# Performance work log

Measured on AMD Instinct MI355X. Metric: run time of the kernel, lower is better.

Reference implementation:

```python
import jax, jax.numpy as jnp
import numpy as np

IN_CH = 2048
OUT_CH = 2048
BATCH = 8192


def setup_inputs() -> dict:
    key = jax.random.key(0)
    ks = jax.random.split(key, 8)
    bound = 1.0 / np.sqrt(IN_CH)  # torch nn.Linear default init range
    inp = {
        "input": jax.random.normal(ks[0], (BATCH, IN_CH), dtype=jnp.float32),
        "hidden": jax.random.normal(ks[1], (BATCH, OUT_CH), dtype=jnp.float32),
        "cell": jax.random.normal(ks[2], (BATCH, OUT_CH), dtype=jnp.float32),
        # Fused gate weights: [IN_CH, 4*OUT_CH] for (forget, input, output, state)
        "W": jax.random.uniform(ks[3], (IN_CH, 4 * OUT_CH), minval=-bound, maxval=bound, dtype=jnp.float32),
        "b": jax.random.uniform(ks[4], (4 * OUT_CH,), minval=-bound, maxval=bound, dtype=jnp.float32),
    }
    return inp


def reference(input, hidden, cell, W, b):
    # One fused GEMM for all four gates, then fused elementwise gate math.
    gates = input @ W + b  # [B, 4*OUT_CH]
    f_g, i_g, o_g, s_g = jnp.split(gates, 4, axis=-1)
    # NOTE: original module applies sigmoid (not tanh) to the state gate.
    forget_gate = jax.nn.sigmoid(f_g)
    input_gate = jax.nn.sigmoid(i_g)
    output_gate = jax.nn.sigmoid(o_g)
    state_gate = jax.nn.sigmoid(s_g)
    new_cell = forget_gate * cell + input_gate * state_gate
    new_hidden = output_gate * jnp.tanh(new_cell)
    return (new_hidden, new_cell)
```

## Files before the change

kernel.cpp:

```cpp
#include <hip/hip_runtime.h>
#include <cstddef>
#include <cstdint>

#define B_ROWS 8192
#define K_DIM  2048
#define N_GATE 2048
#define NG     4
#define W_COLS (NG * N_GATE)

#define BM   256
#define BK   64
#define NTIL 32

typedef __attribute__((ext_vector_type(8))) short s16x8;
typedef __attribute__((ext_vector_type(4))) float f32x4;

__device__ __forceinline__ float fast_sigmoid(float x) {
  return 1.0f / (1.0f + __expf(-x));
}
__device__ __forceinline__ float fast_tanh(float x) {
  return 1.0f - 2.0f / (__expf(2.0f * x) + 1.0f);
}

__global__ void convert_in_kernel(const float4* __restrict__ src,
                                  s16x8* __restrict__ dst, int n8) {
  int idx = blockIdx.x * blockDim.x + threadIdx.x;
  int stride = gridDim.x * blockDim.x;
  for (int i = idx; i < n8; i += stride) {
    float4 a = src[2 * i], b = src[2 * i + 1];
    s16x8 o = { __builtin_bit_cast(short, (__bf16)a.x),
                __builtin_bit_cast(short, (__bf16)a.y),
                __builtin_bit_cast(short, (__bf16)a.z),
                __builtin_bit_cast(short, (__bf16)a.w),
                __builtin_bit_cast(short, (__bf16)b.x),
                __builtin_bit_cast(short, (__bf16)b.y),
                __builtin_bit_cast(short, (__bf16)b.z),
                __builtin_bit_cast(short, (__bf16)b.w) };
    dst[i] = o;
  }
}

__device__ __forceinline__ unsigned int pack2bf16(float x, float y) {
  unsigned short lo = __builtin_bit_cast(unsigned short, (__bf16)x);
  unsigned short hi = __builtin_bit_cast(unsigned short, (__bf16)y);
  return ((unsigned int)hi << 16) | lo;
}

__global__ __launch_bounds__(256) void convert_w_kernel(const float* __restrict__ W,
                                                        short* __restrict__ Wt) {
  __shared__ unsigned int tile[64 * 32];
  const int t = threadIdx.x;
  const int n0 = blockIdx.x * 64;
  const int k0 = blockIdx.y * 64;
  {
    const int kr = t >> 2, seg = t & 3;
    const float4* src = (const float4*)(W + (size_t)(k0 + kr) * W_COLS + n0 + seg * 16);
#pragma unroll
    for (int u = 0; u < 4; ++u) {
      float4 v = src[u];
      const int np = seg * 8 + u * 2;
      tile[kr * 32 + (np ^ (kr & 31))]       = pack2bf16(v.x, v.y);
      tile[kr * 32 + ((np + 1) ^ (kr & 31))] = pack2bf16(v.z, v.w);
    }
  }
  __syncthreads();
  {
    const int np = t >> 3;
    const int kb = t & 7;
    unsigned int w[8];
#pragma unroll
    for (int v = 0; v < 8; ++v) {
      const int k = kb * 8 + v;
      w[v] = tile[k * 32 + (np ^ (k & 31))];
    }
    s16x8 lo, hi;
#pragma unroll
    for (int v = 0; v < 8; ++v) {
      lo[v] = (short)(w[v] & 0xffff);
      hi[v] = (short)(w[v] >> 16);
    }
    short* d0 = Wt + (size_t)(n0 + 2 * np) * K_DIM + k0 + kb * 8;
    *(s16x8*)d0 = lo;
    *(s16x8*)(d0 + K_DIM) = hi;
  }
}

#define GL16(gsrc, ldst)                                                        \
  __builtin_amdgcn_global_load_lds(                                             \
      (const __attribute__((address_space(1))) unsigned int*)(gsrc),            \
      (__attribute__((address_space(3))) unsigned int*)(ldst), 16, 0, 0)

#define MFMA16 __builtin_amdgcn_mfma_f32_16x16x32_bf16

__global__ __launch_bounds__(512, 2) void lstm_gemm_kernel(
    const short* __restrict__ Abf,
    const short* __restrict__ Wt,
    const float* __restrict__ bias,
    const float* __restrict__ cell,
    float* __restrict__ outH,
    float* __restrict__ outC) {
  extern __shared__ short lds[];

  const int tid = threadIdx.x;
  const int lane = tid & 63;
  const int wid = tid >> 6;
  const int wm = wid >> 2;
  const int wn = wid & 3;
  const int lrow = lane & 15;
  const int lk = lane >> 4;

  const int bid = blockIdx.x;
  const int xcd = bid & 7, j = bid >> 3;
  const int tn = xcd * 4 + (j >> 5);
  const int tm = j & 31;
  const int m0 = tm * BM;
  const int n0 = tn * 64;

  size_t a_src[2][2], b_src[2][2];
#pragma unroll
  for (int h = 0; h < 2; ++h)
#pragma unroll
    for (int jj = 0; jj < 2; ++jj) {
      const int p = h * 1024 + jj * 512 + tid;
      const int r = p >> 3;
      const int gl = (p & 7) ^ (r & 7);
      a_src[h][jj] = (size_t)(m0 + r) * K_DIM + gl * 8;
      const int wn16 = r >> 6, g = (r >> 4) & 3, nc4 = r & 15;
      b_src[h][jj] = (size_t)(g * N_GATE + n0 + wn16 * 16 + nc4) * K_DIM + gl * 8;
    }

#define STAGE_A(BUF, H, KT) do {                                                 \
    GL16(Abf + a_src[H][0] + (size_t)(KT) * BK,                                  \
         lds + (BUF) * 16384 + ((H) * 1024 + tid) * 8);                          \
    GL16(Abf + a_src[H][1] + (size_t)(KT) * BK,                                  \
         lds + (BUF) * 16384 + ((H) * 1024 + 512 + tid) * 8);                    \
  } while (0)
#define STAGE_B(BUF, H, KT) do {                                                 \
    GL16(Wt + b_src[H][0] + (size_t)(KT) * BK,                                   \
         lds + 32768 + (BUF) * 16384 + ((H) * 1024 + tid) * 8);                  \
    GL16(Wt + b_src[H][1] + (size_t)(KT) * BK,                                   \
         lds + 32768 + (BUF) * 16384 + ((H) * 1024 + 512 + tid) * 8);            \
  } while (0)

  const int pg0 = (lk ^ (lrow & 7)) * 16;
  const int pg1 = ((4 + lk) ^ (lrow & 7)) * 16;
  const char* aK0 = (const char*)lds + (wm * 128 + lrow) * 128 + pg0;
  const char* aK1 = (const char*)lds + (wm * 128 + lrow) * 128 + pg1;
  const char* bK0 = (const char*)lds + 65536 + (wn * 64 + lrow) * 128 + pg0;
  const char* bK1 = (const char*)lds + 65536 + (wn * 64 + lrow) * 128 + pg1;
#define AF(BUF, MI, KK) (*(const s16x8*)(aK##KK + (BUF) * 32768 + (MI) * 2048))
#define BFR(BUF, G, KK) (*(const s16x8*)(bK##KK + (BUF) * 32768 + (G) * 2048))

  f32x4 acc[8][4];
#pragma unroll
  for (int mi = 0; mi < 8; ++mi)
#pragma unroll
    for (int g = 0; g < 4; ++g) acc[mi][g] = (f32x4){0.f, 0.f, 0.f, 0.f};

  s16x8 bfr[4][2];

#define MMQ(MI, A0, A1) do {                                                     \
    acc[MI][0] = MFMA16(A0, bfr[0][0], acc[MI][0], 0, 0, 0);                     \
    acc[MI][0] = MFMA16(A1, bfr[0][1], acc[MI][0], 0, 0, 0);                     \
    acc[MI][1] = MFMA16(A0, bfr[1][0], acc[MI][1], 0, 0, 0);                     \
    acc[MI][1] = MFMA16(A1, bfr[1][1], acc[MI][1], 0, 0, 0);                     \
    acc[MI][2] = MFMA16(A0, bfr[2][0], acc[MI][2], 0, 0, 0);                     \
    acc[MI][2] = MFMA16(A1, bfr[2][1], acc[MI][2], 0, 0, 0);                     \
    acc[MI][3] = MFMA16(A0, bfr[3][0], acc[MI][3], 0, 0, 0);                     \
    acc[MI][3] = MFMA16(A1, bfr[3][1], acc[MI][3], 0, 0, 0);                     \
  } while (0)

#define VM_NONE do {} while (0)
#define VM_4 asm volatile("s_waitcnt vmcnt(4)" ::: "memory")
#define VM_0 asm volatile("s_waitcnt vmcnt(0)" ::: "memory")

#define PHASE(BUF, Q, LOADB, STG, VM) do {                                       \
    if (LOADB) {                                                                 \
      bfr[0][0] = BFR(BUF, 0, 0); bfr[0][1] = BFR(BUF, 0, 1);                    \
      bfr[1][0] = BFR(BUF, 1, 0); bfr[1][1] = BFR(BUF, 1, 1);                    \
      bfr[2][0] = BFR(BUF, 2, 0); bfr[2][1] = BFR(BUF, 2, 1);                    \
      bfr[3][0] = BFR(BUF, 3, 0); bfr[3][1] = BFR(BUF, 3, 1);                    \
    }                                                                            \
    s16x8 af00 = AF(BUF, 2 * (Q), 0), af01 = AF(BUF, 2 * (Q), 1);                \
    s16x8 af10 = AF(BUF, 2 * (Q) + 1, 0), af11 = AF(BUF, 2 * (Q) + 1, 1);        \
    STG;                                                                         \
    VM;                                                                          \
    __builtin_amdgcn_s_barrier();                                                \
    asm volatile("s_waitcnt lgkmcnt(0)" ::: "memory");                           \
    __builtin_amdgcn_s_setprio(1);                                               \
    MMQ(2 * (Q), af00, af01);                                                    \
    MMQ(2 * (Q) + 1, af10, af11);                                                \
    __builtin_amdgcn_s_setprio(0);                                               \
    __builtin_amdgcn_s_barrier();                                                \
  } while (0)

  STAGE_B(0, 0, 0); STAGE_B(0, 1, 0); STAGE_A(0, 0, 0); STAGE_A(0, 1, 0);
  STAGE_B(1, 0, 1); STAGE_B(1, 1, 1);
  VM_4;
  __builtin_amdgcn_s_barrier();

  for (int i = 0; i < NTIL / 2 - 1; ++i) {
    const int t1 = 2 * i + 1, t2 = 2 * i + 2, t3 = 2 * i + 3;
    PHASE(0, 0, 1, { STAGE_A(1, 0, t1); }, VM_NONE);
    PHASE(0, 1, 0, { STAGE_A(1, 1, t1); }, VM_NONE);
    PHASE(0, 2, 0, { STAGE_B(0, 0, t2); }, VM_NONE);
    PHASE(0, 3, 0, { STAGE_B(0, 1, t2); }, VM_4);
    PHASE(1, 0, 1, { STAGE_A(0, 0, t2); }, VM_NONE);
    PHASE(1, 1, 0, { STAGE_A(0, 1, t2); }, VM_NONE);
    PHASE(1, 2, 0, { STAGE_B(1, 0, t3); }, VM_NONE);
    PHASE(1, 3, 0, { STAGE_B(1, 1, t3); }, VM_4);
  }

  PHASE(0, 0, 1, { STAGE_A(1, 0, 31); }, VM_NONE);
  PHASE(0, 1, 0, { STAGE_A(1, 1, 31); }, VM_NONE);
  PHASE(0, 2, 0, {}, VM_NONE);
  PHASE(0, 3, 0, {}, VM_0);
  PHASE(1, 0, 1, {}, VM_NONE);
  PHASE(1, 1, 0, {}, VM_NONE);
  PHASE(1, 2, 0, {}, VM_NONE);
  PHASE(1, 3, 0, {}, VM_NONE);

  {
    const int n = n0 + wn * 16 + lrow;
    const float b0 = bias[n];
    const float b1 = bias[N_GATE + n];
    const float b2 = bias[2 * N_GATE + n];
    const float b3 = bias[3 * N_GATE + n];
    const size_t base = (size_t)(m0 + wm * 128 + lk * 4) * N_GATE + n;
#pragma unroll
    for (int mi = 0; mi < 8; ++mi) {
#pragma unroll
      for (int r = 0; r < 4; ++r) {
        const size_t off = base + (size_t)(mi * 16 + r) * N_GATE;
        const float fg = fast_sigmoid(acc[mi][0][r] + b0);
        const float ig = fast_sigmoid(acc[mi][1][r] + b1);
        const float og = fast_sigmoid(acc[mi][2][r] + b2);
        const float sg = fast_sigmoid(acc[mi][3][r] + b3);
        const float cn = fg * cell[off] + ig * sg;
        outC[off] = cn;
        outH[off] = og * fast_tanh(cn);
      }
    }
  }
}

extern "C" void kernel_launch(void* const* d_in, const int* in_sizes, int n_in,
                              void* d_out, int out_size, void* d_ws, size_t ws_size,
                              hipStream_t stream) {
  const float* inp  = (const float*)d_in[0];
  const float* cell = (const float*)d_in[2];
  const float* W    = (const float*)d_in[3];
  const float* bias = (const float*)d_in[4];

  float* outH = (float*)d_out;
  float* outC = (float*)d_out + (size_t)B_ROWS * N_GATE;

  short* Abf = (short*)d_ws;
  short* Wt  = (short*)d_ws + (size_t)B_ROWS * K_DIM;

  {
    int n8 = (B_ROWS * K_DIM) / 8;
    convert_in_kernel<<<2048, 256, 0, stream>>>((const float4*)inp,
                                                (s16x8*)Abf, n8);
  }
  {
    dim3 grid(W_COLS / 64, K_DIM / 64);
    convert_w_kernel<<<grid, 256, 0, stream>>>(W, Wt);
  }
  {
    (void)hipFuncSetAttribute(reinterpret_cast<const void*>(&lstm_gemm_kernel),
                              hipFuncAttributeMaxDynamicSharedMemorySize, 131072);
    int nblocks = (B_ROWS / BM) * (N_GATE / 64);
    lstm_gemm_kernel<<<nblocks, 512, 131072, stream>>>(Abf, Wt, bias, cell,
                                                       outH, outC);
  }
}
```

Measured before the change: 536.8 us.

## Triple-buffer A tiles in LDS to deepen the global-load pipeline

Moves the A operand from double to triple buffering in LDS, growing dynamic shared memory to 160KB. A tiles are now prefetched two k-tiles ahead in a rotating buffer, and the wait threshold is relaxed to vmcnt(8). The main loop is restructured into an unrolled three-iteration rotation. The goal is to hide global-load latency for A better, at the cost of more LDS per block and a more intricate buffer schedule.

```diff
diff --git a/kernel.cpp b/kernel.cpp
--- a/kernel.cpp
+++ b/kernel.cpp
@@ -129,27 +129,30 @@
       b_src[h][jj] = (size_t)(g * N_GATE + n0 + wn16 * 16 + nc4) * K_DIM + gl * 8;
     }
 
-#define STAGE_A(BUF, H, KT) do {                                                 \
+#define STAGE_A(AB, H, KT) do {                                                  \
     GL16(Abf + a_src[H][0] + (size_t)(KT) * BK,                                  \
-         lds + (BUF) * 16384 + ((H) * 1024 + tid) * 8);                          \
+         lds + (AB) * 16384 + ((H) * 1024 + tid) * 8);                           \
     GL16(Abf + a_src[H][1] + (size_t)(KT) * BK,                                  \
-         lds + (BUF) * 16384 + ((H) * 1024 + 512 + tid) * 8);                    \
-  } while (0)
-#define STAGE_B(BUF, H, KT) do {                                                 \
+         lds + (AB) * 16384 + ((H) * 1024 + 512 + tid) * 8);                     \
+  } while (0)
+#define STAGE_B(BB, H, KT) do {                                                  \
     GL16(Wt + b_src[H][0] + (size_t)(KT) * BK,                                   \
-         lds + 32768 + (BUF) * 16384 + ((H) * 1024 + tid) * 8);                  \
+         lds + 49152 + (BB) * 16384 + ((H) * 1024 + tid) * 8);                   \
     GL16(Wt + b_src[H][1] + (size_t)(KT) * BK,                                   \
-         lds + 32768 + (BUF) * 16384 + ((H) * 1024 + 512 + tid) * 8);            \
+         lds + 49152 + (BB) * 16384 + ((H) * 1024 + 512 + tid) * 8);             \
   } while (0)
 
   const int pg0 = (lk ^ (lrow & 7)) * 16;
   const int pg1 = ((4 + lk) ^ (lrow & 7)) * 16;
-  const char* aK0 = (const char*)lds + (wm * 128 + lrow) * 128 + pg0;
-  const char* aK1 = (const char*)lds + (wm * 128 + lrow) * 128 + pg1;
-  const char* bK0 = (const char*)lds + 65536 + (wn * 64 + lrow) * 128 + pg0;
-  const char* bK1 = (const char*)lds + 65536 + (wn * 64 + lrow) * 128 + pg1;
-#define AF(BUF, MI, KK) (*(const s16x8*)(aK##KK + (BUF) * 32768 + (MI) * 2048))
-#define BFR(BUF, G, KK) (*(const s16x8*)(bK##KK + (BUF) * 32768 + (G) * 2048))
+  const int aoff0 = (wm * 128 + lrow) * 128 + pg0;
+  const int aoff1 = (wm * 128 + lrow) * 128 + pg1;
+  const int boff0 = (wn * 64 + lrow) * 128 + pg0;
+  const int boff1 = (wn * 64 + lrow) * 128 + pg1;
+  const char* ldsb = (const char*)lds;
+#define AF(AB, MI, KK) \
+  (*(const s16x8*)(ldsb + (AB) * 32768 + aoff##KK + (MI) * 2048))
+#define BFR(BB, G, KK) \
+  (*(const s16x8*)(ldsb + 98304 + (BB) * 32768 + boff##KK + (G) * 2048))
 
   f32x4 acc[8][4];
 #pragma unroll
@@ -171,18 +174,18 @@
   } while (0)
 
 #define VM_NONE do {} while (0)
-#define VM_4 asm volatile("s_waitcnt vmcnt(4)" ::: "memory")
+#define VM_8 asm volatile("s_waitcnt vmcnt(8)" ::: "memory")
 #define VM_0 asm volatile("s_waitcnt vmcnt(0)" ::: "memory")
 
-#define PHASE(BUF, Q, LOADB, STG, VM) do {                                       \
+#define PHASE(AB, BB, Q, LOADB, STG, VM) do {                                    \
     if (LOADB) {                                                                 \
-      bfr[0][0] = BFR(BUF, 0, 0); bfr[0][1] = BFR(BUF, 0, 1);                    \
-      bfr[1][0] = BFR(BUF, 1, 0); bfr[1][1] = BFR(BUF, 1, 1);                    \
-      bfr[2][0] = BFR(BUF, 2, 0); bfr[2][1] = BFR(BUF, 2, 1);                    \
-      bfr[3][0] = BFR(BUF, 3, 0); bfr[3][1] = BFR(BUF, 3, 1);                    \
+      bfr[0][0] = BFR(BB, 0, 0); bfr[0][1] = BFR(BB, 0, 1);                      \
+      bfr[1][0] = BFR(BB, 1, 0); bfr[1][1] = BFR(BB, 1, 1);                      \
+      bfr[2][0] = BFR(BB, 2, 0); bfr[2][1] = BFR(BB, 2, 1);                      \
+      bfr[3][0] = BFR(BB, 3, 0); bfr[3][1] = BFR(BB, 3, 1);                      \
     }                                                                            \
-    s16x8 af00 = AF(BUF, 2 * (Q), 0), af01 = AF(BUF, 2 * (Q), 1);                \
-    s16x8 af10 = AF(BUF, 2 * (Q) + 1, 0), af11 = AF(BUF, 2 * (Q) + 1, 1);        \
+    s16x8 af00 = AF(AB, 2 * (Q), 0), af01 = AF(AB, 2 * (Q), 1);                  \
+    s16x8 af10 = AF(AB, 2 * (Q) + 1, 0), af11 = AF(AB, 2 * (Q) + 1, 1);          \
     STG;                                                                         \
     VM;                                                                          \
     __builtin_amdgcn_s_barrier();                                                \
@@ -194,31 +197,39 @@
     __builtin_amdgcn_s_barrier();                                                \
   } while (0)
 
-  STAGE_B(0, 0, 0); STAGE_B(0, 1, 0); STAGE_A(0, 0, 0); STAGE_A(0, 1, 0);
+#define ITER(RA0, RA1, SA2, SA3, T2, T3) do {                                    \
+    PHASE(RA0, 0, 0, 1, { STAGE_A(SA2, 0, T2); }, VM_NONE);                      \
+    PHASE(RA0, 0, 1, 0, { STAGE_A(SA2, 1, T2); }, VM_NONE);                      \
+    PHASE(RA0, 0, 2, 0, { STAGE_B(0, 0, T2); }, VM_NONE);                        \
+    PHASE(RA0, 0, 3, 0, { STAGE_B(0, 1, T2); }, VM_8);                           \
+    PHASE(RA1, 1, 0, 1, { STAGE_A(SA3, 0, T3); }, VM_NONE);                      \
+    PHASE(RA1, 1, 1, 0, { STAGE_A(SA3, 1, T3); }, VM_NONE);                      \
+    PHASE(RA1, 1, 2, 0, { STAGE_B(1, 0, T3); }, VM_NONE);                        \
+    PHASE(RA1, 1, 3, 0, { STAGE_B(1, 1, T3); }, VM_8);                           \
+  } while (0)
+
+  STAGE_A(0, 0, 0); STAGE_A(0, 1, 0);
+  STAGE_B(0, 0, 0); STAGE_B(0, 1, 0);
+  STAGE_A(1, 0, 1); STAGE_A(1, 1, 1);
   STAGE_B(1, 0, 1); STAGE_B(1, 1, 1);
-  VM_4;
+  VM_8;
   __builtin_amdgcn_s_barrier();
 
-  for (int i = 0; i < NTIL / 2 - 1; ++i) {
-    const int t1 = 2 * i + 1, t2 = 2 * i + 2, t3 = 2 * i + 3;
-    PHASE(0, 0, 1, { STAGE_A(1, 0, t1); }, VM_NONE);
-    PHASE(0, 1, 0, { STAGE_A(1, 1, t1); }, VM_NONE);
-    PHASE(0, 2, 0, { STAGE_B(0, 0, t2); }, VM_NONE);
-    PHASE(0, 3, 0, { STAGE_B(0, 1, t2); }, VM_4);
-    PHASE(1, 0, 1, { STAGE_A(0, 0, t2); }, VM_NONE);
-    PHASE(1, 1, 0, { STAGE_A(0, 1, t2); }, VM_NONE);
-    PHASE(1, 2, 0, { STAGE_B(1, 0, t3); }, VM_NONE);
-    PHASE(1, 3, 0, { STAGE_B(1, 1, t3); }, VM_4);
-  }
-
-  PHASE(0, 0, 1, { STAGE_A(1, 0, 31); }, VM_NONE);
-  PHASE(0, 1, 0, { STAGE_A(1, 1, 31); }, VM_NONE);
-  PHASE(0, 2, 0, {}, VM_NONE);
-  PHASE(0, 3, 0, {}, VM_0);
-  PHASE(1, 0, 1, {}, VM_NONE);
-  PHASE(1, 1, 0, {}, VM_NONE);
-  PHASE(1, 2, 0, {}, VM_NONE);
-  PHASE(1, 3, 0, {}, VM_NONE);
+  for (int o = 0; o < 5; ++o) {
+    const int t = 6 * o;
+    ITER(0, 1, 2, 0, t + 2, t + 3);
+    ITER(2, 0, 1, 2, t + 4, t + 5);
+    ITER(1, 2, 0, 1, t + 6, t + 7);
+  }
+
+  PHASE(0, 0, 0, 1, {}, VM_NONE);
+  PHASE(0, 0, 1, 0, {}, VM_NONE);
+  PHASE(0, 0, 2, 0, {}, VM_NONE);
+  PHASE(0, 0, 3, 0, {}, VM_0);
+  PHASE(1, 1, 0, 1, {}, VM_NONE);
+  PHASE(1, 1, 1, 0, {}, VM_NONE);
+  PHASE(1, 1, 2, 0, {}, VM_NONE);
+  PHASE(1, 1, 3, 0, {}, VM_NONE);
 
   {
     const int n = n0 + wn * 16 + lrow;
@@ -269,9 +280,9 @@
   }
   {
     (void)hipFuncSetAttribute(reinterpret_cast<const void*>(&lstm_gemm_kernel),
-                              hipFuncAttributeMaxDynamicSharedMemorySize, 131072);
+                              hipFuncAttributeMaxDynamicSharedMemorySize, 163840);
     int nblocks = (B_ROWS / BM) * (N_GATE / 64);
-    lstm_gemm_kernel<<<nblocks, 512, 131072, stream>>>(Abf, Wt, bias, cell,
+    lstm_gemm_kernel<<<nblocks, 512, 163840, stream>>>(Abf, Wt, bias, cell,
                                                        outH, outC);
   }
 }
```

After: 534.2 us. About the same (-0.5%).
